# Optimization experiments

Hardware: AMD Instinct MI355X
Metric: run time of the kernel (lower is better)

The kernel has to match this reference:

```python
import jax, jax.numpy as jnp
import numpy as np

D = 768
NH = 8
HD = D // NH
LAT = 64


def layernorm(x, g, b, eps=1e-5):
    mu = x.mean(-1, keepdims=True)
    var = ((x - mu) ** 2).mean(-1, keepdims=True)
    return (x - mu) * jax.lax.rsqrt(var + eps) * g + b


def mha(q, k, v, qw, qb, kw, kb, vw, vb, ow, ob):
    # torch nn.MultiheadAttention (batch_first): Linear is x @ W.T + b
    B, Lq, _ = q.shape
    qh = (q @ qw.T + qb).reshape(B, Lq, NH, HD)
    kh = (k @ kw.T + kb).reshape(B, -1, NH, HD)
    vh = (v @ vw.T + vb).reshape(B, -1, NH, HD)
    s = jnp.einsum('bqhd,bkhd->bhqk', qh, kh) * (1.0 / np.sqrt(HD))
    a = jax.nn.softmax(s, axis=-1)
    o = jnp.einsum('bhqk,bkhd->bqhd', a, vh).reshape(B, Lq, D)
    return o @ ow.T + ob


def setup_inputs() -> dict:
    key = jax.random.key(0)
    ks = jax.random.split(key, 16)
    w = lambda k, shape: (jax.random.normal(k, shape, jnp.float32) * 0.02)
    inp = {
        'frames': jax.random.normal(ks[0], (4, 4, 8, 3, 224, 224), jnp.float32),
        'pe_w': w(ks[1], (D, 3, 14, 14)), 'pe_b': jnp.zeros((D,), jnp.float32),
        'latents': jax.random.normal(ks[2], (LAT, D), jnp.float32),
        'ca_qw': w(ks[3], (D, D)), 'ca_qb': jnp.zeros((D,), jnp.float32),
        'ca_kw': w(ks[4], (D, D)), 'ca_kb': jnp.zeros((D,), jnp.float32),
        'ca_vw': w(ks[5], (D, D)), 'ca_vb': jnp.zeros((D,), jnp.float32),
        'ca_ow': w(ks[6], (D, D)), 'ca_ob': jnp.zeros((D,), jnp.float32),
        'nq_g': jnp.ones((D,), jnp.float32), 'nq_b': jnp.zeros((D,), jnp.float32),
        'nkv_g': jnp.ones((D,), jnp.float32), 'nkv_b': jnp.zeros((D,), jnp.float32),
        'no_g': jnp.ones((D,), jnp.float32), 'no_b': jnp.zeros((D,), jnp.float32),
        'm1_w': w(ks[7], (4 * D, D)), 'm1_b': jnp.zeros((4 * D,), jnp.float32),
        'm2_w': w(ks[8], (D, 4 * D)), 'm2_b': jnp.zeros((D,), jnp.float32),
        'sa_qw': w(ks[9], (D, D)), 'sa_qb': jnp.zeros((D,), jnp.float32),
        'sa_kw': w(ks[10], (D, D)), 'sa_kb': jnp.zeros((D,), jnp.float32),
        'sa_vw': w(ks[11], (D, D)), 'sa_vb': jnp.zeros((D,), jnp.float32),
        'sa_ow': w(ks[12], (D, D)), 'sa_ob': jnp.zeros((D,), jnp.float32),
        'f1_w': w(ks[13], (2 * D, D)), 'f1_b': jnp.zeros((2 * D,), jnp.float32),
        'f2_w': w(ks[14], (D, 2 * D)), 'f2_b': jnp.zeros((D,), jnp.float32),
        'n1_g': jnp.ones((D,), jnp.float32), 'n1_b': jnp.zeros((D,), jnp.float32),
        'n2_g': jnp.ones((D,), jnp.float32), 'n2_b': jnp.zeros((D,), jnp.float32),
    }
    return inp


def reference(frames, pe_w, pe_b, latents, ca_qw, ca_qb, ca_kw, ca_kb, ca_vw, ca_vb,
              ca_ow, ca_ob, nq_g, nq_b, nkv_g, nkv_b, no_g, no_b, m1_w, m1_b, m2_w, m2_b,
              sa_qw, sa_qb, sa_kw, sa_kb, sa_vw, sa_vb, sa_ow, sa_ob, f1_w, f1_b,
              f2_w, f2_b, n1_g, n1_b, n2_g, n2_b):
    B, S, T, C, H, W = frames.shape
    # --- patch embed (Conv2d k=14 s=14), batched over all seconds & frames ---
    f = frames.reshape(B * S * T, C, H, W)
    p = jax.lax.conv_general_dilated(
        f, pe_w, window_strides=(14, 14), padding='VALID',
        dimension_numbers=('NCHW', 'OIHW', 'NCHW')) + pe_b[None, :, None, None]
    npatch = p.shape[2] * p.shape[3]  # 256 patches per frame
    p = p.reshape(B * S * T, D, npatch).transpose(0, 2, 1)  # [BST, P, D]
    kv = p.reshape(B * S, T * npatch, D)  # per-second patch tokens
    # --- Perceiver second tokenizer (loop over seconds == batched over B*S) ---
    q = jnp.broadcast_to(latents[None], (B * S, LAT, D))
    out = mha(layernorm(q, nq_g, nq_b), layernorm(kv, nkv_g, nkv_b), kv,
              ca_qw, ca_qb, ca_kw, ca_kb, ca_vw, ca_vb, ca_ow, ca_ob)
    h = layernorm(out, no_g, no_b)
    tok = out + (jax.nn.gelu(h @ m1_w.T + m1_b) @ m2_w.T + m2_b)
    # concat second tokens along time
    x = tok.reshape(B, S * LAT, D)
    # --- temporal_agg: TransformerEncoderLayer (post-norm, relu, eval mode) ---
    attn = mha(x, x, x, sa_qw, sa_qb, sa_kw, sa_kb, sa_vw, sa_vb, sa_ow, sa_ob)
    x = layernorm(x + attn, n1_g, n1_b)
    ff = jax.nn.relu(x @ f1_w.T + f1_b) @ f2_w.T + f2_b
    x = layernorm(x + ff, n2_g, n2_b)
    return x
```

## Files before the change

kernel.cpp:

```cpp
#include <hip/hip_runtime.h>
#include <hip/hip_bf16.h>
#include <math.h>

typedef __hip_bfloat16 bf16;
typedef __attribute__((ext_vector_type(8))) short short8;
typedef __attribute__((ext_vector_type(4))) float f32x4;

__device__ __forceinline__ void gload16(const bf16* g, bf16* l) {
  __builtin_amdgcn_global_load_lds((const __attribute__((address_space(1))) void*)(g),
                                   (__attribute__((address_space(3))) void*)(l), 16, 0, 0);
}

struct Seg { const float* src; bf16* dst; int rows, sc, dc; };
struct Segs { Seg s[13]; };

__global__ __launch_bounds__(256) void prepack_kernel(Segs segs) {
  Seg sg = segs.s[blockIdx.y];
  long long total = (long long)sg.rows * sg.dc;
  for (long long idx = (long long)blockIdx.x * 256 + threadIdx.x; idx < total;
       idx += (long long)gridDim.x * 256) {
    int r = (int)(idx / sg.dc), c = (int)(idx % sg.dc);
    float v = (c < sg.sc) ? sg.src[(long long)r * sg.sc + c] : 0.f;
    sg.dst[idx] = __float2bfloat16(v);
  }
}

__global__ __launch_bounds__(256) void concat3_kernel(const float* __restrict__ a,
                                                      const float* __restrict__ b,
                                                      const float* __restrict__ c,
                                                      float* __restrict__ o) {
  int i = blockIdx.x * 256 + threadIdx.x;
  if (i < 2304)
    o[i] = i < 768 ? a[i] : (i < 1536 ? b[i - 768] : c[i - 1536]);
}

__global__ __launch_bounds__(256) void im2col_kernel(const float* __restrict__ frames,
                                                     bf16* __restrict__ out) {
  unsigned idx = blockIdx.x * 256u + threadIdx.x;
  unsigned k = idx % 608u;
  unsigned m = idx / 608u;
  float v = 0.f;
  if (k < 588u) {
    unsigned n = m >> 8;
    unsigned p = m & 255u;
    unsigned py = p >> 4, px = p & 15u;
    unsigned c = k / 196u, r = k % 196u;
    unsigned i = r / 14u, j = r % 14u;
    v = frames[((n * 3u + c) * 224u + (py * 14u + i)) * 224u + (px * 14u + j)];
  }
  out[idx] = __float2bfloat16(v);
}

__global__ __launch_bounds__(256) void ln_kernel(const float* __restrict__ inF,
                                                 const bf16* __restrict__ inB,
                                                 const float* __restrict__ g,
                                                 const float* __restrict__ b,
                                                 float* __restrict__ outF,
                                                 bf16* __restrict__ outB,
                                                 int validRows) {
  int row = blockIdx.x;
  int tid = threadIdx.x;
  __shared__ float red[8];
  size_t base = (size_t)row * 768;
  if (row >= validRows) {
    for (int i = 0; i < 3; ++i) {
      int c = tid + i * 256;
      if (outB) outB[base + c] = __float2bfloat16(0.f);
      if (outF) outF[base + c] = 0.f;
    }
    return;
  }
  float x[3];
  for (int i = 0; i < 3; ++i) {
    int c = tid + i * 256;
    x[i] = inF ? inF[base + c] : __bfloat162float(inB[base + c]);
  }
  float s = x[0] + x[1] + x[2];
  float sq = x[0] * x[0] + x[1] * x[1] + x[2] * x[2];
  for (int off = 32; off; off >>= 1) {
    s += __shfl_down(s, off);
    sq += __shfl_down(sq, off);
  }
  int w = tid >> 6;
  if ((tid & 63) == 0) { red[w] = s; red[4 + w] = sq; }
  __syncthreads();
  if (tid == 0) {
    red[0] = red[0] + red[1] + red[2] + red[3];
    red[4] = red[4] + red[5] + red[6] + red[7];
  }
  __syncthreads();
  float mean = red[0] * (1.f / 768.f);
  float var = red[4] * (1.f / 768.f) - mean * mean;
  float rs = rsqrtf(var + 1e-5f);
  for (int i = 0; i < 3; ++i) {
    int c = tid + i * 256;
    float y = (x[i] - mean) * rs * g[c] + b[c];
    if (outF) outF[base + c] = y;
    if (outB) outB[base + c] = __float2bfloat16(y);
  }
}

__global__ __launch_bounds__(256) void gemm_bf16(
    const bf16* __restrict__ A, const bf16* __restrict__ Bw,
    const float* __restrict__ bias, const float* __restrict__ resid,
    float* __restrict__ outF, bf16* __restrict__ outB,
    int M, int N, int K, int act) {
  __shared__ bf16 As[128 * 32];
  __shared__ bf16 Bs[128 * 32];
  int tid = threadIdx.x;
  int m0 = blockIdx.y * 128, n0 = blockIdx.x * 128;
  int lane = tid & 63, w = tid >> 6;
  int wr = w >> 1, wc = w & 1;
  int l15 = lane & 15, lq = lane >> 4;
  int srow = lane >> 2, scol = (lane & 3) * 8;
  const bf16* Abase = A + (size_t)m0 * K;
  const bf16* Bbase = Bw + (size_t)n0 * K;
  f32x4 acc[4][4] = {};

  for (int kt = 0; kt < K; kt += 32) {
    #pragma unroll
    for (int i = 0; i < 2; ++i) {
      int seg = w * 2 + i;
      int row = seg * 16 + srow;
      gload16(Abase + (size_t)row * K + kt + scol, &As[seg * 512]);
      gload16(Bbase + (size_t)row * K + kt + scol, &Bs[seg * 512]);
    }
    __syncthreads();
    short8 af[4], bfrag[4];
    #pragma unroll
    for (int mi = 0; mi < 4; ++mi)
      af[mi] = *(const short8*)(&As[(wr * 64 + mi * 16 + l15) * 32 + lq * 8]);
    #pragma unroll
    for (int ni = 0; ni < 4; ++ni)
      bfrag[ni] = *(const short8*)(&Bs[(wc * 64 + ni * 16 + l15) * 32 + lq * 8]);
    #pragma unroll
    for (int mi = 0; mi < 4; ++mi)
      #pragma unroll
      for (int ni = 0; ni < 4; ++ni)
        acc[mi][ni] = __builtin_amdgcn_mfma_f32_16x16x32_bf16(af[mi], bfrag[ni],
                                                              acc[mi][ni], 0, 0, 0);
    __syncthreads();
  }

  #pragma unroll
  for (int mi = 0; mi < 4; ++mi)
    #pragma unroll
    for (int ni = 0; ni < 4; ++ni) {
      int col = n0 + wc * 64 + ni * 16 + l15;
      float bv = bias ? bias[col] : 0.f;
      #pragma unroll
      for (int j = 0; j < 4; ++j) {
        int row = m0 + wr * 64 + mi * 16 + lq * 4 + j;
        float v = acc[mi][ni][j] + bv;
        if (act == 1) {
          float x = v;
          v = 0.5f * x * (1.f + tanhf(0.79788456080286535f * (x + 0.044715f * x * x * x)));
        } else if (act == 2) {
          v = fmaxf(v, 0.f);
        }
        size_t idx = (size_t)row * N + col;
        if (resid) v += resid[idx];
        if (outF) outF[idx] = v;
        if (outB) outB[idx] = __float2bfloat16(v);
      }
    }
}

__global__ __launch_bounds__(256) void flash_kernel(
    const bf16* __restrict__ Q, const bf16* __restrict__ Kp,
    const bf16* __restrict__ V, bf16* __restrict__ O,
    int Lk, int qRPB, int kRPB, int oRPB, int ld) {
  const float scale = 0.10206207261596575f;
  __shared__ bf16 Vt[96 * 72];
  __shared__ bf16 Ps[4 * 16 * 72];
  int tid = threadIdx.x, lane = tid & 63, w = tid >> 6;
  int l15 = lane & 15, lq = lane >> 4;
  int b = blockIdx.z, h = blockIdx.y, qt = blockIdx.x;
  int qbase = b * qRPB + qt * 64 + w * 16;
  int kbase = b * kRPB;
  int obase = b * oRPB + qt * 64 + w * 16;
  int ch = h * 96;

  short8 aQ[3];
  #pragma unroll
  for (int kd = 0; kd < 3; ++kd)
    aQ[kd] = *(const short8*)(Q + (size_t)(qbase + l15) * ld + ch + kd * 32 + lq * 8);

  f32x4 oacc[6] = {};
  float mrun[4] = {-1e30f, -1e30f, -1e30f, -1e30f};
  float lrun[4] = {0.f, 0.f, 0.f, 0.f};

  for (int kc = 0; kc < Lk; kc += 64) {
    for (int u = tid; u < 768; u += 256) {
      int kk = u / 12, dc = u % 12;
      short8 v = *(const short8*)(V + (size_t)(kbase + kc + kk) * ld + ch + dc * 8);
      const bf16* pv = (const bf16*)&v;
      #pragma unroll
      for (int e = 0; e < 8; ++e) Vt[(dc * 8 + e) * 72 + kk] = pv[e];
    }
    __syncthreads();

    f32x4 sacc[4] = {};
    #pragma unroll
    for (int ni = 0; ni < 4; ++ni)
      #pragma unroll
      for (int kd = 0; kd < 3; ++kd) {
        short8 bK = *(const short8*)(Kp + (size_t)(kbase + kc + ni * 16 + l15) * ld +
                                     ch + kd * 32 + lq * 8);
        sacc[ni] = __builtin_amdgcn_mfma_f32_16x16x32_bf16(aQ[kd], bK, sacc[ni], 0, 0, 0);
      }
    #pragma unroll
    for (int ni = 0; ni < 4; ++ni)
      #pragma unroll
      for (int j = 0; j < 4; ++j) sacc[ni][j] *= scale;

    float al[4];
    #pragma unroll
    for (int j = 0; j < 4; ++j) {
      float mx = fmaxf(fmaxf(sacc[0][j], sacc[1][j]), fmaxf(sacc[2][j], sacc[3][j]));
      #pragma unroll
      for (int off = 1; off < 16; off <<= 1) mx = fmaxf(mx, __shfl_xor(mx, off));
      float mnew = fmaxf(mrun[j], mx);
      float alpha = __expf(mrun[j] - mnew);
      float rs = 0.f;
      #pragma unroll
      for (int ni = 0; ni < 4; ++ni) {
        float p = __expf(sacc[ni][j] - mnew);
        sacc[ni][j] = p;
        rs += p;
      }
      #pragma unroll
      for (int off = 1; off < 16; off <<= 1) rs += __shfl_xor(rs, off);
      lrun[j] = lrun[j] * alpha + rs;
      mrun[j] = mnew;
      al[j] = alpha;
    }

    #pragma unroll
    for (int ni = 0; ni < 4; ++ni)
      #pragma unroll
      for (int j = 0; j < 4; ++j)
        Ps[(w * 16 + lq * 4 + j) * 72 + ni * 16 + l15] = __float2bfloat16(sacc[ni][j]);
    #pragma unroll
    for (int t = 0; t < 6; ++t)
      #pragma unroll
      for (int j = 0; j < 4; ++j) oacc[t][j] *= al[j];
    short8 aP[2];
    #pragma unroll
    for (int ks = 0; ks < 2; ++ks)
      aP[ks] = *(const short8*)(&Ps[(w * 16 + l15) * 72 + ks * 32 + lq * 8]);
    #pragma unroll
    for (int t = 0; t < 6; ++t)
      #pragma unroll
      for (int ks = 0; ks < 2; ++ks) {
        short8 bV = *(const short8*)(&Vt[(t * 16 + l15) * 72 + ks * 32 + lq * 8]);
        oacc[t] = __builtin_amdgcn_mfma_f32_16x16x32_bf16(aP[ks], bV, oacc[t], 0, 0, 0);
      }
    __syncthreads();
  }

  #pragma unroll
  for (int t = 0; t < 6; ++t)
    #pragma unroll
    for (int j = 0; j < 4; ++j) {
      int row = obase + lq * 4 + j;
      int col = ch + t * 16 + l15;
      O[(size_t)row * 768 + col] = __float2bfloat16(oacc[t][j] / lrun[j]);
    }
}

__global__ __launch_bounds__(256) void flash_split_kernel(
    const bf16* __restrict__ Q, const bf16* __restrict__ Kp,
    const bf16* __restrict__ V, float* __restrict__ Opart,
    float* __restrict__ Mpart, float* __restrict__ Lpart,
    int splitLen, int kRPB) {
  const float scale = 0.10206207261596575f;
  __shared__ bf16 Vt[96 * 72];
  __shared__ bf16 Ps[4 * 16 * 72];
  int tid = threadIdx.x, lane = tid & 63, w = tid >> 6;
  int l15 = lane & 15, lq = lane >> 4;
  int s = blockIdx.x, h = blockIdx.y, b = blockIdx.z;
  int kbase = b * kRPB + s * splitLen;
  int ch = h * 96;

  short8 aQ[3];
  #pragma unroll
  for (int kd = 0; kd < 3; ++kd)
    aQ[kd] = *(const short8*)(Q + (size_t)(w * 16 + l15) * 768 + ch + kd * 32 + lq * 8);

  f32x4 oacc[6] = {};
  float mrun[4] = {-1e30f, -1e30f, -1e30f, -1e30f};
  float lrun[4] = {0.f, 0.f, 0.f, 0.f};

  for (int kc = 0; kc < splitLen; kc += 64) {
    for (int u = tid; u < 768; u += 256) {
      int kk = u / 12, dc = u % 12;
      short8 v = *(const short8*)(V + (size_t)(kbase + kc + kk) * 768 + ch + dc * 8);
      const bf16* pv = (const bf16*)&v;
      #pragma unroll
      for (int e = 0; e < 8; ++e) Vt[(dc * 8 + e) * 72 + kk] = pv[e];
    }
    __syncthreads();

    f32x4 sacc[4] = {};
    #pragma unroll
    for (int ni = 0; ni < 4; ++ni)
      #pragma unroll
      for (int kd = 0; kd < 3; ++kd) {
        short8 bK = *(const short8*)(Kp + (size_t)(kbase + kc + ni * 16 + l15) * 768 +
                                     ch + kd * 32 + lq * 8);
        sacc[ni] = __builtin_amdgcn_mfma_f32_16x16x32_bf16(aQ[kd], bK, sacc[ni], 0, 0, 0);
      }
    #pragma unroll
    for (int ni = 0; ni < 4; ++ni)
      #pragma unroll
      for (int j = 0; j < 4; ++j) sacc[ni][j] *= scale;

    float al[4];
    #pragma unroll
    for (int j = 0; j < 4; ++j) {
      float mx = fmaxf(fmaxf(sacc[0][j], sacc[1][j]), fmaxf(sacc[2][j], sacc[3][j]));
      #pragma unroll
      for (int off = 1; off < 16; off <<= 1) mx = fmaxf(mx, __shfl_xor(mx, off));
      float mnew = fmaxf(mrun[j], mx);
      float alpha = __expf(mrun[j] - mnew);
      float rs = 0.f;
      #pragma unroll
      for (int ni = 0; ni < 4; ++ni) {
        float p = __expf(sacc[ni][j] - mnew);
        sacc[ni][j] = p;
        rs += p;
      }
      #pragma unroll
      for (int off = 1; off < 16; off <<= 1) rs += __shfl_xor(rs, off);
      lrun[j] = lrun[j] * alpha + rs;
      mrun[j] = mnew;
      al[j] = alpha;
    }

    #pragma unroll
    for (int ni = 0; ni < 4; ++ni)
      #pragma unroll
      for (int j = 0; j < 4; ++j)
        Ps[(w * 16 + lq * 4 + j) * 72 + ni * 16 + l15] = __float2bfloat16(sacc[ni][j]);
    #pragma unroll
    for (int t = 0; t < 6; ++t)
      #pragma unroll
      for (int j = 0; j < 4; ++j) oacc[t][j] *= al[j];
    short8 aP[2];
    #pragma unroll
    for (int ks = 0; ks < 2; ++ks)
      aP[ks] = *(const short8*)(&Ps[(w * 16 + l15) * 72 + ks * 32 + lq * 8]);
    #pragma unroll
    for (int t = 0; t < 6; ++t)
      #pragma unroll
      for (int ks = 0; ks < 2; ++ks) {
        short8 bV = *(const short8*)(&Vt[(t * 16 + l15) * 72 + ks * 32 + lq * 8]);
        oacc[t] = __builtin_amdgcn_mfma_f32_16x16x32_bf16(aP[ks], bV, oacc[t], 0, 0, 0);
      }
    __syncthreads();
  }

  int orow = b * 64 + w * 16;
  #pragma unroll
  for (int t = 0; t < 6; ++t)
    #pragma unroll
    for (int j = 0; j < 4; ++j)
      Opart[(size_t)(s * 1024 + orow + lq * 4 + j) * 768 + ch + t * 16 + l15] = oacc[t][j];
  if (l15 == 0) {
    #pragma unroll
    for (int j = 0; j < 4; ++j) {
      int qq = w * 16 + lq * 4 + j;
      int mi = ((s * 16 + b) * 8 + h) * 64 + qq;
      Mpart[mi] = mrun[j];
      Lpart[mi] = lrun[j];
    }
  }
}

__global__ __launch_bounds__(256) void flash_merge_kernel(
    const float* __restrict__ Opart, const float* __restrict__ Mpart,
    const float* __restrict__ Lpart, bf16* __restrict__ O, int nsplit) {
  int row = blockIdx.x;
  int tid = threadIdx.x;
  int c0 = tid * 3;
  int b = row >> 6, q = row & 63;
  int h = c0 / 96;
  float m = -1e30f;
  for (int s = 0; s < nsplit; ++s)
    m = fmaxf(m, Mpart[((s * 16 + b) * 8 + h) * 64 + q]);
  float l = 0.f, o0 = 0.f, o1 = 0.f, o2 = 0.f;
  for (int s = 0; s < nsplit; ++s) {
    int mi = ((s * 16 + b) * 8 + h) * 64 + q;
    float ws = __expf(Mpart[mi] - m);
    l += ws * Lpart[mi];
    const float* op = Opart + (size_t)(s * 1024 + row) * 768 + c0;
    o0 += ws * op[0]; o1 += ws * op[1]; o2 += ws * op[2];
  }
  float inv = 1.f / l;
  size_t ob = (size_t)row * 768 + c0;
  O[ob]     = __float2bfloat16(o0 * inv);
  O[ob + 1] = __float2bfloat16(o1 * inv);
  O[ob + 2] = __float2bfloat16(o2 * inv);
}

extern "C" void kernel_launch(void* const* d_in, const int* in_sizes, int n_in,
                              void* d_out, int out_size, void* d_ws, size_t ws_size,
                              hipStream_t stream) {
  const float* frames = (const float*)d_in[0];
  const float* pe_w   = (const float*)d_in[1];
  const float* pe_b   = (const float*)d_in[2];
  const float* latents= (const float*)d_in[3];
  const float* ca_qw  = (const float*)d_in[4];  const float* ca_qb = (const float*)d_in[5];
  const float* ca_kw  = (const float*)d_in[6];  const float* ca_kb = (const float*)d_in[7];
  const float* ca_vw  = (const float*)d_in[8];  const float* ca_vb = (const float*)d_in[9];
  const float* ca_ow  = (const float*)d_in[10]; const float* ca_ob = (const float*)d_in[11];
  const float* nq_g   = (const float*)d_in[12]; const float* nq_b  = (const float*)d_in[13];
  const float* nkv_g  = (const float*)d_in[14]; const float* nkv_b = (const float*)d_in[15];
  const float* no_g   = (const float*)d_in[16]; const float* no_b  = (const float*)d_in[17];
  const float* m1_w   = (const float*)d_in[18]; const float* m1_b  = (const float*)d_in[19];
  const float* m2_w   = (const float*)d_in[20]; const float* m2_b  = (const float*)d_in[21];
  const float* sa_qw  = (const float*)d_in[22]; const float* sa_qb = (const float*)d_in[23];
  const float* sa_kw  = (const float*)d_in[24]; const float* sa_kb = (const float*)d_in[25];
  const float* sa_vw  = (const float*)d_in[26]; const float* sa_vb = (const float*)d_in[27];
  const float* sa_ow  = (const float*)d_in[28]; const float* sa_ob = (const float*)d_in[29];
  const float* f1_w   = (const float*)d_in[30]; const float* f1_b  = (const float*)d_in[31];
  const float* f2_w   = (const float*)d_in[32]; const float* f2_b  = (const float*)d_in[33];
  const float* n1_g   = (const float*)d_in[34]; const float* n1_b  = (const float*)d_in[35];
  const float* n2_g   = (const float*)d_in[36]; const float* n2_b  = (const float*)d_in[37];

  char* ws = (char*)d_ws;
  size_t off = 0;
  auto take = [&](size_t bytes) -> char* {
    char* p = ws + off;
    off += (bytes + 255) & ~(size_t)255;
    return p;
  };

  bf16* w_pe  = (bf16*)take((size_t)768 * 608 * 2);
  bf16* w_caq = (bf16*)take((size_t)768 * 768 * 2);
  bf16* w_cak = (bf16*)take((size_t)768 * 768 * 2);
  bf16* w_cav = (bf16*)take((size_t)768 * 768 * 2);
  bf16* w_cao = (bf16*)take((size_t)768 * 768 * 2);
  bf16* w_m1  = (bf16*)take((size_t)3072 * 768 * 2);
  bf16* w_m2  = (bf16*)take((size_t)768 * 3072 * 2);
  bf16* w_saq = (bf16*)take((size_t)768 * 768 * 2);
  bf16* w_sak = (bf16*)take((size_t)768 * 768 * 2);
  bf16* w_sav = (bf16*)take((size_t)768 * 768 * 2);
  bf16* w_sao = (bf16*)take((size_t)768 * 768 * 2);
  bf16* w_f1  = (bf16*)take((size_t)1536 * 768 * 2);
  bf16* w_f2  = (bf16*)take((size_t)768 * 1536 * 2);
  float* sab_cat = (float*)take((size_t)2304 * 4);

  bf16* q_ln = (bf16*)take((size_t)128 * 768 * 2);
  bf16* qh   = (bf16*)take((size_t)128 * 768 * 2);

  bf16* kv = (bf16*)take((size_t)32768 * 768 * 2);
  bf16* vh = (bf16*)take((size_t)32768 * 768 * 2);
  bf16* kh = (bf16*)take((size_t)32768 * 768 * 2);

  const size_t REGION = (size_t)32768 * 608 * 2;
  char* region = take(REGION);
  bf16*  imcol = (bf16*)region;
  float* Opart = (float*)region;
  float* Mpart = (float*)(region + 25165824);
  float* Lpart = (float*)(region + 25165824 + 262144);
  bf16*  attn_o = (bf16*)(region + REGION - (size_t)1024 * 768 * 2);
  size_t ro = 0;
  auto rtake = [&](size_t bytes) -> char* {
    char* p = region + ro;
    ro += (bytes + 255) & ~(size_t)255;
    return p;
  };
  float* out_f  = (float*)rtake((size_t)1024 * 768 * 4);
  bf16*  h_b    = (bf16*)rtake((size_t)1024 * 768 * 2);
  bf16*  g_b    = (bf16*)rtake((size_t)1024 * 3072 * 2);
  float* tok_f  = (float*)rtake((size_t)1024 * 768 * 4);
  bf16*  tok_b  = (bf16*)rtake((size_t)1024 * 768 * 2);
  bf16*  xqkv   = (bf16*)rtake((size_t)1024 * 2304 * 2);
  bf16*  sa_o   = (bf16*)rtake((size_t)1024 * 768 * 2);
  float* y_f    = (float*)rtake((size_t)1024 * 768 * 4);
  float* x1f    = (float*)rtake((size_t)1024 * 768 * 4);
  bf16*  x1b    = (bf16*)rtake((size_t)1024 * 768 * 2);
  bf16*  ff1    = (bf16*)rtake((size_t)1024 * 1536 * 2);
  float* z_f    = (float*)rtake((size_t)1024 * 768 * 4);
  (void)ws_size; (void)in_sizes; (void)n_in; (void)out_size;

  Segs segs;
  segs.s[0]  = {pe_w,  w_pe,  768, 588, 608};
  segs.s[1]  = {ca_qw, w_caq, 768, 768, 768};
  segs.s[2]  = {ca_kw, w_cak, 768, 768, 768};
  segs.s[3]  = {ca_vw, w_cav, 768, 768, 768};
  segs.s[4]  = {ca_ow, w_cao, 768, 768, 768};
  segs.s[5]  = {m1_w,  w_m1,  3072, 768, 768};
  segs.s[6]  = {m2_w,  w_m2,  768, 3072, 3072};
  segs.s[7]  = {sa_qw, w_saq, 768, 768, 768};
  segs.s[8]  = {sa_kw, w_sak, 768, 768, 768};
  segs.s[9]  = {sa_vw, w_sav, 768, 768, 768};
  segs.s[10] = {f1_w,  w_f1,  1536, 768, 768};
  segs.s[11] = {f2_w,  w_f2,  768, 1536, 1536};
  segs.s[12] = {sa_ow, w_sao, 768, 768, 768};
  prepack_kernel<<<dim3(2304, 13), 256, 0, stream>>>(segs);
  concat3_kernel<<<9, 256, 0, stream>>>(sa_qb, sa_kb, sa_vb, sab_cat);

  ln_kernel<<<128, 256, 0, stream>>>(latents, nullptr, nq_g, nq_b, nullptr, q_ln, 64);

  im2col_kernel<<<77824, 256, 0, stream>>>(frames, imcol);

  gemm_bf16<<<dim3(6, 256), 256, 0, stream>>>(imcol, w_pe, pe_b, nullptr, nullptr, kv,
                                              32768, 768, 608, 0);

  gemm_bf16<<<dim3(6, 1), 256, 0, stream>>>(q_ln, w_caq, ca_qb, nullptr, nullptr, qh,
                                            128, 768, 768, 0);

  gemm_bf16<<<dim3(6, 256), 256, 0, stream>>>(kv, w_cav, ca_vb, nullptr, nullptr, vh,
                                              32768, 768, 768, 0);

  ln_kernel<<<32768, 256, 0, stream>>>(nullptr, kv, nkv_g, nkv_b, nullptr, kv, 32768);

  gemm_bf16<<<dim3(6, 256), 256, 0, stream>>>(kv, w_cak, ca_kb, nullptr, nullptr, kh,
                                              32768, 768, 768, 0);

  flash_split_kernel<<<dim3(8, 8, 16), 256, 0, stream>>>(qh, kh, vh, Opart, Mpart, Lpart,
                                                         256, 2048);
  flash_merge_kernel<<<1024, 256, 0, stream>>>(Opart, Mpart, Lpart, attn_o, 8);

  gemm_bf16<<<dim3(6, 8), 256, 0, stream>>>(attn_o, w_cao, ca_ob, nullptr, out_f, nullptr,
                                            1024, 768, 768, 0);

  ln_kernel<<<1024, 256, 0, stream>>>(out_f, nullptr, no_g, no_b, nullptr, h_b, 1024);

  gemm_bf16<<<dim3(24, 8), 256, 0, stream>>>(h_b, w_m1, m1_b, nullptr, nullptr, g_b,
                                             1024, 3072, 768, 1);

  gemm_bf16<<<dim3(6, 8), 256, 0, stream>>>(g_b, w_m2, m2_b, out_f, tok_f, tok_b,
                                            1024, 768, 3072, 0);

  gemm_bf16<<<dim3(18, 8), 256, 0, stream>>>(tok_b, w_saq, sab_cat, nullptr, nullptr, xqkv,
                                             1024, 2304, 768, 0);

  flash_kernel<<<dim3(4, 8, 4), 256, 0, stream>>>(xqkv, xqkv + 768, xqkv + 1536, sa_o,
                                                  256, 256, 256, 256, 2304);

  gemm_bf16<<<dim3(6, 8), 256, 0, stream>>>(sa_o, w_sao, sa_ob, tok_f, y_f, nullptr,
                                            1024, 768, 768, 0);

  ln_kernel<<<1024, 256, 0, stream>>>(y_f, nullptr, n1_g, n1_b, x1f, x1b, 1024);

  gemm_bf16<<<dim3(12, 8), 256, 0, stream>>>(x1b, w_f1, f1_b, nullptr, nullptr, ff1,
                                             1024, 1536, 768, 2);

  gemm_bf16<<<dim3(6, 8), 256, 0, stream>>>(ff1, w_f2, f2_b, x1f, z_f, nullptr,
                                            1024, 768, 1536, 0);

  ln_kernel<<<1024, 256, 0, stream>>>(z_f, nullptr, n2_g, n2_b, (float*)d_out, nullptr, 1024);
}
```

Baseline: 761.7 us.

## Fold KV layernorm into fused K/V GEMM and double-buffer GEMM tiles

```diff
diff --git a/kernel.cpp b/kernel.cpp
--- a/kernel.cpp
+++ b/kernel.cpp
@@ -10,8 +10,11 @@
   __builtin_amdgcn_global_load_lds((const __attribute__((address_space(1))) void*)(g),
                                    (__attribute__((address_space(3))) void*)(l), 16, 0, 0);
 }
-
-struct Seg { const float* src; bf16* dst; int rows, sc, dc; };
+__device__ __forceinline__ float bfu2f(unsigned short u) {
+  union { unsigned u; float f; } c; c.u = ((unsigned)u) << 16; return c.f;
+}
+
+struct Seg { const float* src; bf16* dst; int rows, sc, dc; const float* scale; };
 struct Segs { Seg s[13]; };
 
 __global__ __launch_bounds__(256) void prepack_kernel(Segs segs) {
@@ -21,6 +24,7 @@
        idx += (long long)gridDim.x * 256) {
     int r = (int)(idx / sg.dc), c = (int)(idx % sg.dc);
     float v = (c < sg.sc) ? sg.src[(long long)r * sg.sc + c] : 0.f;
+    if (sg.scale && c < sg.sc) v *= sg.scale[c];
     sg.dst[idx] = __float2bfloat16(v);
   }
 }
@@ -32,6 +36,57 @@
   int i = blockIdx.x * 256 + threadIdx.x;
   if (i < 2304)
     o[i] = i < 768 ? a[i] : (i < 1536 ? b[i - 768] : c[i - 1536]);
+}
+
+__global__ __launch_bounds__(256) void s12_kernel(const float* __restrict__ kw,
+                                                  const float* __restrict__ g,
+                                                  const float* __restrict__ b,
+                                                  const float* __restrict__ kb,
+                                                  float* __restrict__ s1,
+                                                  float* __restrict__ s2) {
+  int j = blockIdx.x;
+  int tid = threadIdx.x;
+  const float* wr_ = kw + (size_t)j * 768;
+  float a = 0.f, c = 0.f;
+  #pragma unroll
+  for (int i = 0; i < 3; ++i) {
+    int d = tid + i * 256;
+    float wv = wr_[d];
+    a += wv * g[d];
+    c += wv * b[d];
+  }
+  __shared__ float red[16];
+  for (int off = 32; off; off >>= 1) { a += __shfl_down(a, off); c += __shfl_down(c, off); }
+  int w = tid >> 6;
+  if ((tid & 63) == 0) { red[w] = a; red[8 + w] = c; }
+  __syncthreads();
+  if (tid == 0) {
+    s1[j] = red[0] + red[1] + red[2] + red[3];
+    s2[j] = red[8] + red[9] + red[10] + red[11] + kb[j];
+  }
+}
+
+__global__ __launch_bounds__(256) void rowstats_kernel(const bf16* __restrict__ x,
+                                                       float* __restrict__ mu,
+                                                       float* __restrict__ rs) {
+  int row = blockIdx.x * 4 + (threadIdx.x >> 6);
+  int lane = threadIdx.x & 63;
+  const unsigned short* p = (const unsigned short*)(x + (size_t)row * 768);
+  float s = 0.f, sq = 0.f;
+  #pragma unroll
+  for (int i = 0; i < 3; ++i) {
+    ushort4 v = *(const ushort4*)(p + lane * 4 + i * 256);
+    float f0 = bfu2f(v.x), f1 = bfu2f(v.y), f2 = bfu2f(v.z), f3 = bfu2f(v.w);
+    s += f0 + f1 + f2 + f3;
+    sq += f0 * f0 + f1 * f1 + f2 * f2 + f3 * f3;
+  }
+  for (int off = 32; off; off >>= 1) { s += __shfl_down(s, off); sq += __shfl_down(sq, off); }
+  if (lane == 0) {
+    float m = s * (1.f / 768.f);
+    float var = sq * (1.f / 768.f) - m * m;
+    mu[row] = m;
+    rs[row] = rsqrtf(var + 1e-5f);
+  }
 }
 
 __global__ __launch_bounds__(256) void im2col_kernel(const float* __restrict__ frames,
@@ -104,42 +159,98 @@
     const bf16* __restrict__ A, const bf16* __restrict__ Bw,
     const float* __restrict__ bias, const float* __restrict__ resid,
     float* __restrict__ outF, bf16* __restrict__ outB,
-    int M, int N, int K, int act) {
-  __shared__ bf16 As[128 * 32];
-  __shared__ bf16 Bs[128 * 32];
+    int M, int N, int K, int act,
+    const float* __restrict__ rowMu, const float* __restrict__ rowRs,
+    const float* __restrict__ s1, const float* __restrict__ s2,
+    bf16* __restrict__ outB2) {
+  __shared__ bf16 As[2][4096];
+  __shared__ bf16 Bs[2][4096];
   int tid = threadIdx.x;
-  int m0 = blockIdx.y * 128, n0 = blockIdx.x * 128;
+  int nwg = gridDim.x * gridDim.y;
+  int orig = blockIdx.y * gridDim.x + blockIdx.x;
+  int xcd = orig & 7, loc = orig >> 3;
+  int qq = nwg >> 3, rr = nwg & 7;
+  int swz = (xcd < rr) ? (xcd * (qq + 1) + loc) : (rr * (qq + 1) + (xcd - rr) * qq + loc);
+  int m0 = (swz / gridDim.x) * 128, n0 = (swz % gridDim.x) * 128;
+
   int lane = tid & 63, w = tid >> 6;
   int wr = w >> 1, wc = w & 1;
   int l15 = lane & 15, lq = lane >> 4;
-  int srow = lane >> 2, scol = (lane & 3) * 8;
-  const bf16* Abase = A + (size_t)m0 * K;
-  const bf16* Bbase = Bw + (size_t)n0 * K;
+  const bf16* Abase = A + (size_t)m0 * K + w * 8;
+  const bf16* Bbase = Bw + (size_t)n0 * K + w * 8;
   f32x4 acc[4][4] = {};
 
-  for (int kt = 0; kt < K; kt += 32) {
-    #pragma unroll
-    for (int i = 0; i < 2; ++i) {
-      int seg = w * 2 + i;
-      int row = seg * 16 + srow;
-      gload16(Abase + (size_t)row * K + kt + scol, &As[seg * 512]);
-      gload16(Bbase + (size_t)row * K + kt + scol, &Bs[seg * 512]);
-    }
-    __syncthreads();
-    short8 af[4], bfrag[4];
+  int nt = K >> 5;
+  #pragma unroll
+  for (int i = 0; i < 2; ++i) {
+    int r = i * 64 + lane;
+    gload16(Abase + (size_t)r * K, &As[0][(w * 2 + i) * 512]);
+    gload16(Bbase + (size_t)r * K, &Bs[0][(w * 2 + i) * 512]);
+  }
+  for (int t = 0; t < nt; ++t) {
+    int cur = t & 1;
+    if (t + 1 < nt) {
+      int kt = (t + 1) << 5;
+      #pragma unroll
+      for (int i = 0; i < 2; ++i) {
+        int r = i * 64 + lane;
+        gload16(Abase + (size_t)r * K + kt, &As[cur ^ 1][(w * 2 + i) * 512]);
+        gload16(Bbase + (size_t)r * K + kt, &Bs[cur ^ 1][(w * 2 + i) * 512]);
+      }
+      asm volatile("s_waitcnt vmcnt(4)" ::: "memory");
+    } else {
+      asm volatile("s_waitcnt vmcnt(0)" ::: "memory");
+    }
+    __builtin_amdgcn_s_barrier();
+    asm volatile("" ::: "memory");
+    const bf16* Ab = &As[cur][lq * 1024];
+    const bf16* Bb = &Bs[cur][lq * 1024];
+    short8 af[4], bfr[4];
     #pragma unroll
     for (int mi = 0; mi < 4; ++mi)
-      af[mi] = *(const short8*)(&As[(wr * 64 + mi * 16 + l15) * 32 + lq * 8]);
+      af[mi] = *(const short8*)(Ab + (wr * 64 + mi * 16 + l15) * 8);
     #pragma unroll
     for (int ni = 0; ni < 4; ++ni)
-      bfrag[ni] = *(const short8*)(&Bs[(wc * 64 + ni * 16 + l15) * 32 + lq * 8]);
+      bfr[ni] = *(const short8*)(Bb + (wc * 64 + ni * 16 + l15) * 8);
+    __builtin_amdgcn_s_setprio(1);
     #pragma unroll
     for (int mi = 0; mi < 4; ++mi)
       #pragma unroll
       for (int ni = 0; ni < 4; ++ni)
-        acc[mi][ni] = __builtin_amdgcn_mfma_f32_16x16x32_bf16(af[mi], bfrag[ni],
+        acc[mi][ni] = __builtin_amdgcn_mfma_f32_16x16x32_bf16(af[mi], bfr[ni],
                                                               acc[mi][ni], 0, 0, 0);
-    __syncthreads();
+    __builtin_amdgcn_s_setprio(0);
+    asm volatile("" ::: "memory");
+    __builtin_amdgcn_s_barrier();
+  }
+
+  if (act == 3) {
+    #pragma unroll
+    for (int ni = 0; ni < 4; ++ni) {
+      int col = n0 + wc * 64 + ni * 16 + l15;
+      if (col < 768) {
+        float bv = bias[col];
+        #pragma unroll
+        for (int mi = 0; mi < 4; ++mi)
+          #pragma unroll
+          for (int j = 0; j < 4; ++j) {
+            int row = m0 + wr * 64 + mi * 16 + lq * 4 + j;
+            outB[(size_t)row * 768 + col] = __float2bfloat16(acc[mi][ni][j] + bv);
+          }
+      } else {
+        int ck = col - 768;
+        float a1 = s1[ck], a2 = s2[ck];
+        #pragma unroll
+        for (int mi = 0; mi < 4; ++mi)
+          #pragma unroll
+          for (int j = 0; j < 4; ++j) {
+            int row = m0 + wr * 64 + mi * 16 + lq * 4 + j;
+            float v = rowRs[row] * (acc[mi][ni][j] - rowMu[row] * a1) + a2;
+            outB2[(size_t)row * 768 + ck] = __float2bfloat16(v);
+          }
+      }
+    }
+    return;
   }
 
   #pragma unroll
@@ -222,16 +333,16 @@
       for (int off = 1; off < 16; off <<= 1) mx = fmaxf(mx, __shfl_xor(mx, off));
       float mnew = fmaxf(mrun[j], mx);
       float alpha = __expf(mrun[j] - mnew);
-      float rs = 0.f;
+      float rsum = 0.f;
       #pragma unroll
       for (int ni = 0; ni < 4; ++ni) {
         float p = __expf(sacc[ni][j] - mnew);
         sacc[ni][j] = p;
-        rs += p;
-      }
-      #pragma unroll
-      for (int off = 1; off < 16; off <<= 1) rs += __shfl_xor(rs, off);
-      lrun[j] = lrun[j] * alpha + rs;
+        rsum += p;
+      }
+      #pragma unroll
+      for (int off = 1; off < 16; off <<= 1) rsum += __shfl_xor(rsum, off);
+      lrun[j] = lrun[j] * alpha + rsum;
       mrun[j] = mnew;
       al[j] = alpha;
     }
@@ -324,16 +435,16 @@
       for (int off = 1; off < 16; off <<= 1) mx = fmaxf(mx, __shfl_xor(mx, off));
       float mnew = fmaxf(mrun[j], mx);
       float alpha = __expf(mrun[j] - mnew);
-      float rs = 0.f;
+      float rsum = 0.f;
       #pragma unroll
       for (int ni = 0; ni < 4; ++ni) {
         float p = __expf(sacc[ni][j] - mnew);
         sacc[ni][j] = p;
-        rs += p;
-      }
-      #pragma unroll
-      for (int off = 1; off < 16; off <<= 1) rs += __shfl_xor(rs, off);
-      lrun[j] = lrun[j] * alpha + rs;
+        rsum += p;
+      }
+      #pragma unroll
+      for (int off = 1; off < 16; off <<= 1) rsum += __shfl_xor(rsum, off);
+      lrun[j] = lrun[j] * alpha + rsum;
       mrun[j] = mnew;
       al[j] = alpha;
     }
@@ -370,8 +481,8 @@
   if (l15 == 0) {
     #pragma unroll
     for (int j = 0; j < 4; ++j) {
-      int qq = w * 16 + lq * 4 + j;
-      int mi = ((s * 16 + b) * 8 + h) * 64 + qq;
+      int qqi = w * 16 + lq * 4 + j;
+      int mi = ((s * 16 + b) * 8 + h) * 64 + qqi;
       Mpart[mi] = mrun[j];
       Lpart[mi] = lrun[j];
     }
@@ -437,20 +548,23 @@
     return p;
   };
 
-  bf16* w_pe  = (bf16*)take((size_t)768 * 608 * 2);
-  bf16* w_caq = (bf16*)take((size_t)768 * 768 * 2);
-  bf16* w_cak = (bf16*)take((size_t)768 * 768 * 2);
-  bf16* w_cav = (bf16*)take((size_t)768 * 768 * 2);
-  bf16* w_cao = (bf16*)take((size_t)768 * 768 * 2);
-  bf16* w_m1  = (bf16*)take((size_t)3072 * 768 * 2);
-  bf16* w_m2  = (bf16*)take((size_t)768 * 3072 * 2);
-  bf16* w_saq = (bf16*)take((size_t)768 * 768 * 2);
-  bf16* w_sak = (bf16*)take((size_t)768 * 768 * 2);
-  bf16* w_sav = (bf16*)take((size_t)768 * 768 * 2);
-  bf16* w_sao = (bf16*)take((size_t)768 * 768 * 2);
-  bf16* w_f1  = (bf16*)take((size_t)1536 * 768 * 2);
-  bf16* w_f2  = (bf16*)take((size_t)768 * 1536 * 2);
+  bf16* w_pe   = (bf16*)take((size_t)768 * 608 * 2);
+  bf16* w_caq  = (bf16*)take((size_t)768 * 768 * 2);
+  bf16* w_cakv = (bf16*)take((size_t)1536 * 768 * 2);
+  bf16* w_cao  = (bf16*)take((size_t)768 * 768 * 2);
+  bf16* w_m1   = (bf16*)take((size_t)3072 * 768 * 2);
+  bf16* w_m2   = (bf16*)take((size_t)768 * 3072 * 2);
+  bf16* w_saq  = (bf16*)take((size_t)768 * 768 * 2);
+  bf16* w_sak  = (bf16*)take((size_t)768 * 768 * 2);
+  bf16* w_sav  = (bf16*)take((size_t)768 * 768 * 2);
+  bf16* w_sao  = (bf16*)take((size_t)768 * 768 * 2);
+  bf16* w_f1   = (bf16*)take((size_t)1536 * 768 * 2);
+  bf16* w_f2   = (bf16*)take((size_t)768 * 1536 * 2);
   float* sab_cat = (float*)take((size_t)2304 * 4);
+  float* s1v  = (float*)take((size_t)768 * 4);
+  float* s2v  = (float*)take((size_t)768 * 4);
+  float* muv  = (float*)take((size_t)32768 * 4);
+  float* rsv  = (float*)take((size_t)32768 * 4);
 
   bf16* q_ln = (bf16*)take((size_t)128 * 768 * 2);
   bf16* qh   = (bf16*)take((size_t)128 * 768 * 2);
@@ -487,71 +601,79 @@
   (void)ws_size; (void)in_sizes; (void)n_in; (void)out_size;
 
   Segs segs;
-  segs.s[0]  = {pe_w,  w_pe,  768, 588, 608};
-  segs.s[1]  = {ca_qw, w_caq, 768, 768, 768};
-  segs.s[2]  = {ca_kw, w_cak, 768, 768, 768};
-  segs.s[3]  = {ca_vw, w_cav, 768, 768, 768};
-  segs.s[4]  = {ca_ow, w_cao, 768, 768, 768};
-  segs.s[5]  = {m1_w,  w_m1,  3072, 768, 768};
-  segs.s[6]  = {m2_w,  w_m2,  768, 3072, 3072};
-  segs.s[7]  = {sa_qw, w_saq, 768, 768, 768};
-  segs.s[8]  = {sa_kw, w_sak, 768, 768, 768};
-  segs.s[9]  = {sa_vw, w_sav, 768, 768, 768};
-  segs.s[10] = {f1_w,  w_f1,  1536, 768, 768};
-  segs.s[11] = {f2_w,  w_f2,  768, 1536, 1536};
-  segs.s[12] = {sa_ow, w_sao, 768, 768, 768};
+  segs.s[0]  = {pe_w,  w_pe,  768, 588, 608, nullptr};
+  segs.s[1]  = {ca_qw, w_caq, 768, 768, 768, nullptr};
+  segs.s[2]  = {ca_vw, w_cakv, 768, 768, 768, nullptr};
+  segs.s[3]  = {ca_kw, w_cakv + (size_t)768 * 768, 768, 768, 768, nkv_g};
+  segs.s[4]  = {ca_ow, w_cao, 768, 768, 768, nullptr};
+  segs.s[5]  = {m1_w,  w_m1,  3072, 768, 768, nullptr};
+  segs.s[6]  = {m2_w,  w_m2,  768, 3072, 3072, nullptr};
+  segs.s[7]  = {sa_qw, w_saq, 768, 768, 768, nullptr};
+  segs.s[8]  = {sa_kw, w_sak, 768, 768, 768, nullptr};
+  segs.s[9]  = {sa_vw, w_sav, 768, 768, 768, nullptr};
+  segs.s[10] = {f1_w,  w_f1,  1536, 768, 768, nullptr};
+  segs.s[11] = {f2_w,  w_f2,  768, 1536, 1536, nullptr};
+  segs.s[12] = {sa_ow, w_sao, 768, 768, 768, nullptr};
   prepack_kernel<<<dim3(2304, 13), 256, 0, stream>>>(segs);
   concat3_kernel<<<9, 256, 0, stream>>>(sa_qb, sa_kb, sa_vb, sab_cat);
+  s12_kernel<<<768, 256, 0, stream>>>(ca_kw, nkv_g, nkv_b, ca_kb, s1v, s2v);
 
   ln_kernel<<<128, 256, 0, stream>>>(latents, nullptr, nq_g, nq_b, nullptr, q_ln, 64);
 
   im2col_kernel<<<77824, 256, 0, stream>>>(frames, imcol);
 
   gemm_bf16<<<dim3(6, 256), 256, 0, stream>>>(imcol, w_pe, pe_b, nullptr, nullptr, kv,
-                                              32768, 768, 608, 0);
+                                              32768, 768, 608, 0,
+                                              nullptr, nullptr, nullptr, nullptr, nullptr);
 
   gemm_bf16<<<dim3(6, 1), 256, 0, stream>>>(q_ln, w_caq, ca_qb, nullptr, nullptr, qh,
-                                            128, 768, 768, 0);
-
-  gemm_bf16<<<dim3(6, 256), 256, 0, stream>>>(kv, w_cav, ca_vb, nullptr, nullptr, vh,
-                                              32768, 768, 768, 0);
-
-  ln_kernel<<<32768, 256, 0, stream>>>(nullptr, kv, nkv_g, nkv_b, nullptr, kv, 32768);
-
-  gemm_bf16<<<dim3(6, 256), 256, 0, stream>>>(kv, w_cak, ca_kb, nullptr, nullptr, kh,
-                                              32768, 768, 768, 0);
+                                            128, 768, 768, 0,
+                                            nullptr, nullptr, nullptr, nullptr, nullptr);
+
+  rowstats_kernel<<<8192, 256, 0, stream>>>(kv, muv, rsv);
+
+  gemm_bf16<<<dim3(12, 256), 256, 0, stream>>>(kv, w_cakv, ca_vb, nullptr, nullptr, vh,
+                                               32768, 1536, 768, 3,
+                                               muv, rsv, s1v, s2v, kh);
 
   flash_split_kernel<<<dim3(8, 8, 16), 256, 0, stream>>>(qh, kh, vh, Opart, Mpart, Lpart,
                                                          256, 2048);
   flash_merge_kernel<<<1024, 256, 0, stream>>>(Opart, Mpart, Lpart, attn_o, 8);
 
   gemm_bf16<<<dim3(6, 8), 256, 0, stream>>>(attn_o, w_cao, ca_ob, nullptr, out_f, nullptr,
-                                            1024, 768, 768, 0);
+                                            1024, 768, 768, 0,
+                                            nullptr, nullptr, nullptr, nullptr, nullptr);
 
   ln_kernel<<<1024, 256, 0, stream>>>(out_f, nullptr, no_g, no_b, nullptr, h_b, 1024);
 
   gemm_bf16<<<dim3(24, 8), 256, 0, stream>>>(h_b, w_m1, m1_b, nullptr, nullptr, g_b,
-                                             1024, 3072, 768, 1);
+                                             1024, 3072, 768, 1,
+                                             nullptr, nullptr, nullptr, nullptr, nullptr);
 
   gemm_bf16<<<dim3(6, 8), 256, 0, stream>>>(g_b, w_m2, m2_b, out_f, tok_f, tok_b,
-                                            1024, 768, 3072, 0);
+                                            1024, 768, 3072, 0,
+                                            nullptr, nullptr, nullptr, nullptr, nullptr);
 
   gemm_bf16<<<dim3(18, 8), 256, 0, stream>>>(tok_b, w_saq, sab_cat, nullptr, nullptr, xqkv,
-                                             1024, 2304, 768, 0);
+                                             1024, 2304, 768, 0,
+                                             nullptr, nullptr, nullptr, nullptr, nullptr);
 
   flash_kernel<<<dim3(4, 8, 4), 256, 0, stream>>>(xqkv, xqkv + 768, xqkv + 1536, sa_o,
                                                   256, 256, 256, 256, 2304);
 
   gemm_bf16<<<dim3(6, 8), 256, 0, stream>>>(sa_o, w_sao, sa_ob, tok_f, y_f, nullptr,
-                                            1024, 768, 768, 0);
+                                            1024, 768, 768, 0,
+                                            nullptr, nullptr, nullptr, nullptr, nullptr);
 
   ln_kernel<<<1024, 256, 0, stream>>>(y_f, nullptr, n1_g, n1_b, x1f, x1b, 1024);
 
   gemm_bf16<<<dim3(12, 8), 256, 0, stream>>>(x1b, w_f1, f1_b, nullptr, nullptr, ff1,
-                                             1024, 1536, 768, 2);
+                                             1024, 1536, 768, 2,
+                                             nullptr, nullptr, nullptr, nullptr, nullptr);
 
   gemm_bf16<<<dim3(6, 8), 256, 0, stream>>>(ff1, w_f2, f2_b, x1f, z_f, nullptr,
-                                            1024, 768, 1536, 0);
+                                            1024, 768, 1536, 0,
+                                            nullptr, nullptr, nullptr, nullptr, nullptr);
 
   ln_kernel<<<1024, 256, 0, stream>>>(z_f, nullptr, n2_g, n2_b, (float*)d_out, nullptr, 1024);
 }
```

Measured after the change: 819.5 us. 7.6% more time.
